# Kernel optimization log

Hardware: AMD Instinct MI355X
Metric: run time of the kernel (lower is better)

The kernel has to match this reference:

```python
import jax, jax.numpy as jnp
import numpy as np

DIM = 1024
SEQ_LEN = 4096
K_RANK = 256
HEADS = 16
HEAD_DIM = DIM // HEADS
BATCH = 4


def setup_inputs() -> dict:
    key = jax.random.key(0)
    k1, k2, k3, k4 = jax.random.split(key, 4)
    x = jax.random.normal(k1, (BATCH, SEQ_LEN, DIM), dtype=jnp.float32)
    W_qkv = jax.random.normal(k2, (DIM, 3 * DIM), dtype=jnp.float32) * (DIM ** -0.5)
    E = jax.random.normal(k3, (SEQ_LEN, K_RANK), dtype=jnp.float32)
    W_out = jax.random.normal(k4, (DIM, DIM), dtype=jnp.float32) * (DIM ** -0.5)
    b_out = jnp.zeros((DIM,), dtype=jnp.float32)
    return {"x": x, "W_qkv": W_qkv, "E": E, "W_out": W_out, "b_out": b_out}


def reference(x, W_qkv, E, W_out, b_out):
    B, N, D = x.shape
    scale = HEAD_DIM ** -0.5
    qkv = x @ W_qkv                                    # [B, N, 3D]
    q, k, v = jnp.split(qkv, 3, axis=-1)
    # [B, N, D] -> [B, H, N, hd]
    reshape_heads = lambda t: t.reshape(B, N, HEADS, HEAD_DIM).transpose(0, 2, 1, 3)
    q, k, v = map(reshape_heads, (q, k, v))
    # Linformer low-rank projection along sequence: [B, H, N, hd] -> [B, H, k, hd]
    k_proj = jnp.einsum('bhnd,nk->bhkd', k, E)
    v_proj = jnp.einsum('bhnd,nk->bhkd', v, E)
    scores = jnp.einsum('bhnd,bhkd->bhnk', q, k_proj) * scale  # [B, H, N, k]
    attn = jax.nn.softmax(scores, axis=-1)
    out = jnp.einsum('bhnk,bhkd->bhnd', attn, v_proj)  # [B, H, N, hd]
    out = out.transpose(0, 2, 1, 3).reshape(B, N, D)
    return out @ W_out + b_out
```

## Files before the change

### kernel.cpp

```cpp
#include <hip/hip_runtime.h>
#include <hip/hip_bf16.h>

typedef _Float16 f16;
typedef __attribute__((ext_vector_type(4))) _Float16 f16x4;
typedef __attribute__((ext_vector_type(8))) _Float16 f16x8;
typedef __attribute__((ext_vector_type(4))) float f32x4;

#define DIM 1024
#define SEQ 4096
#define KRNK 256
#define NH 16
#define HD 64
#define NB 4
#define ROWS (NB*SEQ)
#define NSPLIT 4

typedef const void __attribute__((address_space(1))) as1cv;
typedef void __attribute__((address_space(3))) as3v;

static __device__ __forceinline__ void glds16(const void* g, void* l) {
  __builtin_amdgcn_global_load_lds((as1cv*)g, (as3v*)l, 16, 0, 0);
}

template<int MODE>
__global__ __launch_bounds__(256) void k_prep_w(const float* __restrict__ in,
                                                f16* __restrict__ oh, f16* __restrict__ ol,
                                                int R, int C) {
  __shared__ float tile[64][65];
  int rtiles = R >> 6;
  int rt = blockIdx.x % rtiles, ct = blockIdx.x / rtiles;
  int r0 = rt << 6, c0 = ct << 6, t = threadIdx.x;
#pragma unroll
  for (int i = 0; i < 16; ++i) {
    int e = t + i * 256; int r = e >> 6, c = e & 63;
    tile[r][c] = in[(size_t)(r0 + r) * C + c0 + c];
  }
  __syncthreads();
#pragma unroll
  for (int i = 0; i < 16; ++i) {
    int e = t + i * 256; int c = e >> 6, r = e & 63;
    float v = tile[r][c];
    size_t idx = (size_t)(c0 + c) * R + r0 + r;
    if constexpr (MODE == 0) {
      v *= 256.0f;
      f16 h = (f16)v;
      oh[idx] = h;
      ol[idx] = (f16)(v - (float)h);
    } else {
      oh[idx] = (f16)v;
    }
  }
}

template<bool WH>
__global__ __launch_bounds__(256) void k_tsplit(const float* __restrict__ in,
                                                f16* __restrict__ oh,
                                                f16* __restrict__ oth,
                                                int R, int C) {
  __shared__ float tile[64][65];
  int rtiles = R >> 6;
  int rt = blockIdx.x % rtiles, ct = blockIdx.x / rtiles;
  int r0 = rt << 6, c0 = ct << 6, t = threadIdx.x;
  int cq = (t & 15) * 4, rr = t >> 4;
#pragma unroll
  for (int i = 0; i < 4; ++i) {
    int r = rr + i * 16;
    f32x4 v = *(const f32x4*)&in[(size_t)(r0 + r) * C + c0 + cq];
    tile[r][cq] = v[0]; tile[r][cq + 1] = v[1];
    tile[r][cq + 2] = v[2]; tile[r][cq + 3] = v[3];
    if constexpr (WH) {
      f16x4 h = {(f16)v[0], (f16)v[1], (f16)v[2], (f16)v[3]};
      *(f16x4*)&oh[(size_t)(r0 + r) * C + c0 + cq] = h;
    }
  }
  __syncthreads();
  int d4 = (t >> 4) * 4, sq = (t & 15) * 4;
#pragma unroll
  for (int j = 0; j < 4; ++j) {
    f16x4 h4;
#pragma unroll
    for (int k = 0; k < 4; ++k) h4[k] = (f16)tile[sq + k][d4 + j];
    *(f16x4*)&oth[(size_t)(c0 + d4 + j) * R + r0 + sq] = h4;
  }
}

template<bool ASPL, bool BSPL, int MT, int NT>
static __device__ __forceinline__ void mm_core(
    const f16* __restrict__ Ah, const f16* __restrict__ Al, int lda,
    const f16* __restrict__ Bh, const f16* __restrict__ Bl, int ldb,
    int bm, int bn, int K,
    f16* sAh, f16* sAl, f16* sBh, f16* sBl,
    f32x4 (&acc)[MT / 32][NT / 32]) {
  constexpr int MREP = MT / 32, NREP = NT / 32;
  constexpr int AI = MT / 32, BI = NT / 32;
  constexpr int ASZ = MT * 64, BSZ = NT * 64;
  const int t = threadIdx.x;
  const int lane = t & 63, w = t >> 6;
  const int wr = w >> 1, wc = w & 1;
  const int l15 = lane & 15, hi = lane >> 4;
  const f32x4 zero = {0.f, 0.f, 0.f, 0.f};
#pragma unroll
  for (int m = 0; m < MREP; ++m)
#pragma unroll
    for (int n = 0; n < NREP; ++n) acc[m][n] = zero;

  auto stage = [&](int kk, int bufi) {
#pragma unroll
    for (int i = 0; i < AI; ++i) {
      int c = t + i * 256;
      int row = c >> 3, cc = c & 7;
      size_t g = (size_t)(bm + row) * lda + kk + cc * 8;
      glds16(Ah + g, &sAh[bufi * ASZ + c * 8]);
      if constexpr (ASPL) glds16(Al + g, &sAl[bufi * ASZ + c * 8]);
    }
#pragma unroll
    for (int i = 0; i < BI; ++i) {
      int c = t + i * 256;
      int row = c >> 3, cc = c & 7;
      size_t g = (size_t)(bn + row) * ldb + kk + cc * 8;
      glds16(Bh + g, &sBh[bufi * BSZ + c * 8]);
      if constexpr (BSPL) glds16(Bl + g, &sBl[bufi * BSZ + c * 8]);
    }
  };

  stage(0, 0);
  int cur = 0;
  for (int kk = 0; kk < K; kk += 64) {
    __syncthreads();
    if (kk + 64 < K) stage(kk + 64, cur ^ 1);

    f16x8 avh[MREP][2], avl[MREP][2], bvh[NREP][2], bvl[NREP][2];
#pragma unroll
    for (int m = 0; m < MREP; ++m)
#pragma unroll
      for (int ks = 0; ks < 2; ++ks) {
        int off = cur * ASZ + (wr * (MT / 2) + m * 16 + l15) * 64 + ks * 32 + hi * 8;
        avh[m][ks] = *(const f16x8*)&sAh[off];
        if constexpr (ASPL) avl[m][ks] = *(const f16x8*)&sAl[off];
      }
#pragma unroll
    for (int n = 0; n < NREP; ++n)
#pragma unroll
      for (int ks = 0; ks < 2; ++ks) {
        int off = cur * BSZ + (wc * (NT / 2) + n * 16 + l15) * 64 + ks * 32 + hi * 8;
        bvh[n][ks] = *(const f16x8*)&sBh[off];
        if constexpr (BSPL) bvl[n][ks] = *(const f16x8*)&sBl[off];
      }
#pragma unroll
    for (int m = 0; m < MREP; ++m)
#pragma unroll
      for (int n = 0; n < NREP; ++n)
#pragma unroll
        for (int ks = 0; ks < 2; ++ks) {
          if constexpr (ASPL && BSPL) {
            acc[m][n] = __builtin_amdgcn_mfma_f32_16x16x32_f16(avl[m][ks], bvh[n][ks], acc[m][n], 0, 0, 0);
            acc[m][n] = __builtin_amdgcn_mfma_f32_16x16x32_f16(avh[m][ks], bvl[n][ks], acc[m][n], 0, 0, 0);
          } else if constexpr (BSPL) {
            acc[m][n] = __builtin_amdgcn_mfma_f32_16x16x32_f16(avh[m][ks], bvl[n][ks], acc[m][n], 0, 0, 0);
          }
          acc[m][n] = __builtin_amdgcn_mfma_f32_16x16x32_f16(avh[m][ks], bvh[n][ks], acc[m][n], 0, 0, 0);
        }
    cur ^= 1;
  }
}

__global__ __launch_bounds__(256) void k_xe2(const f16* __restrict__ Eth,
                                             const f16* __restrict__ xth,
                                             float* __restrict__ XEp) {
  __shared__ __align__(16) f16 sA[2 * 128 * 64];
  __shared__ __align__(16) f16 sB[2 * 64 * 64];
  int bx = blockIdx.x;
  int nt = bx & 15, mt = (bx >> 4) & 1, b = (bx >> 5) & 3, sp = bx >> 7;
  int bm = mt << 7, bn = nt << 6;
  int koff = sp * (SEQ / NSPLIT);
  f32x4 acc[4][2];
  mm_core<false, false, 128, 64>(Eth + koff, nullptr, SEQ,
                                 xth + (size_t)b * SEQ + koff, nullptr, ROWS,
                                 bm, bn, SEQ / NSPLIT, sA, nullptr, sB, nullptr, acc);
  const int t = threadIdx.x, lane = t & 63, w = t >> 6;
  const int wr = w >> 1, wc = w & 1, l15 = lane & 15, hi = lane >> 4;
#pragma unroll
  for (int m = 0; m < 4; ++m)
#pragma unroll
    for (int n = 0; n < 2; ++n)
#pragma unroll
      for (int r = 0; r < 4; ++r) {
        int kr = bm + wr * 64 + m * 16 + hi * 4 + r;
        int dd = bn + wc * 32 + n * 16 + l15;
        XEp[(((size_t)sp * NB + b) * KRNK + kr) * DIM + dd] = acc[m][n][r];
      }
}

__global__ __launch_bounds__(256) void k_xered(const float* __restrict__ XEp,
                                               f16* __restrict__ XEh,
                                               f16* __restrict__ XEl) {
  size_t i = (size_t)blockIdx.x * 256 + threadIdx.x;
  const size_t sstride = (size_t)NB * KRNK * DIM / 4;
  const f32x4* p = (const f32x4*)XEp;
  f32x4 s = p[i];
#pragma unroll
  for (int sp = 1; sp < NSPLIT; ++sp) s += p[i + sp * sstride];
  f16x4 h4, l4;
#pragma unroll
  for (int j = 0; j < 4; ++j) {
    f16 h = (f16)s[j];
    h4[j] = h;
    l4[j] = (f16)(s[j] - (float)h);
  }
  *(f16x4*)&XEh[i * 4] = h4;
  *(f16x4*)&XEl[i * 4] = l4;
}

static __device__ __forceinline__ void go_map(int bx, int& bm, int& bn) {
  int xcd = bx & 7, idx = bx >> 3;
  int nt = idx & 7, mt = xcd * 32 + (idx >> 3);
  bm = mt << 6;
  bn = nt << 7;
}

__global__ __launch_bounds__(256) void k_gq(const f16* __restrict__ xh,
                                            const f16* __restrict__ Wph,
                                            f16* __restrict__ q) {
  __shared__ __align__(16) f16 sA[2 * 64 * 64];
  __shared__ __align__(16) f16 sB[2 * 128 * 64];
  int bm, bn;
  go_map(blockIdx.x, bm, bn);
  f32x4 acc[2][4];
  mm_core<false, false, 64, 128>(xh, nullptr, DIM, Wph, nullptr, DIM, bm, bn, DIM,
                                 sA, nullptr, sB, nullptr, acc);
  const int t = threadIdx.x, lane = t & 63, w = t >> 6;
  const int wr = w >> 1, wc = w & 1, l15 = lane & 15, hi = lane >> 4;
#pragma unroll
  for (int m = 0; m < 2; ++m)
#pragma unroll
    for (int n = 0; n < 4; ++n)
#pragma unroll
      for (int r = 0; r < 4; ++r) {
        int row = bm + wr * 32 + m * 16 + hi * 4 + r;
        int col = bn + wc * 64 + n * 16 + l15;
        q[(size_t)row * DIM + col] = (f16)(acc[m][n][r] * (1.0f / 256.0f));
      }
}

__global__ __launch_bounds__(256) void k_t2(const f16* __restrict__ XEh,
                                            const f16* __restrict__ XEl,
                                            const f16* __restrict__ Wph,
                                            const f16* __restrict__ Wpl,
                                            f16* __restrict__ kph,
                                            f16* __restrict__ vpt) {
  __shared__ __align__(16) f16 sAh[2 * 128 * 64], sAl[2 * 128 * 64];
  __shared__ __align__(16) f16 sBh[2 * 64 * 64], sBl[2 * 64 * 64];
  int bx = blockIdx.x;
  int nt = bx & 15, mt = (bx >> 4) & 1, b = (bx >> 5) & 3, kv = bx >> 7;
  size_t abase = (size_t)b * KRNK * DIM;
  size_t wbase = (size_t)(DIM + kv * DIM) * DIM;
  f32x4 acc[4][2];
  mm_core<true, true, 128, 64>(XEh + abase, XEl + abase, DIM, Wph + wbase, Wpl + wbase, DIM,
                               mt << 7, nt << 6, DIM, sAh, sAl, sBh, sBl, acc);
  const int t = threadIdx.x, lane = t & 63, w = t >> 6;
  const int wr = w >> 1, wc = w & 1, l15 = lane & 15, hi = lane >> 4;
#pragma unroll
  for (int m = 0; m < 4; ++m)
#pragma unroll
    for (int n = 0; n < 2; ++n)
#pragma unroll
      for (int r = 0; r < 4; ++r) {
        int row = (mt << 7) + wr * 64 + m * 16 + hi * 4 + r;
        int col = (nt << 6) + wc * 32 + n * 16 + l15;
        float s = acc[m][n][r] * (1.0f / 256.0f);
        if (!kv) kph[((size_t)(b * KRNK + row)) * DIM + col] = (f16)s;
        else     vpt[((size_t)(b * DIM + col)) * KRNK + row] = (f16)s;
      }
}

__global__ __launch_bounds__(256) void k_attn(const f16* __restrict__ q,
                                              const f16* __restrict__ kph,
                                              const f16* __restrict__ vpt,
                                              f16* __restrict__ oattn) {
  __shared__ __align__(16) f16 sBuf[2][64 * 64];
  __shared__ __align__(16) f16 sP[64 * KRNK];
  int bx0 = blockIdx.x;
  int swz = (bx0 & 7) * 512 + (bx0 >> 3);
  int qb = swz & 63;
  int bh = swz >> 6;
  int b = bh >> 4, h = bh & 15;
  int t = threadIdx.x;
  int lane = t & 63, w = t >> 6;
  int l15 = lane & 15, hi = lane >> 4;

  const f16* kbase = kph + ((size_t)(b * KRNK)) * DIM + h * HD;
  const f16* vbase = vpt + ((size_t)(b * DIM + h * HD)) * KRNK;

  auto stageK = [&](int c, int bufi) {
#pragma unroll
    for (int i = 0; i < 2; ++i) {
      int sid = w * 128 + i * 64 + lane;
      int kr = sid >> 3, sl = sid & 7;
      glds16(kbase + (size_t)(c * 64 + kr) * DIM + ((sl ^ (kr & 7)) * 8),
             &sBuf[bufi][sid * 8]);
    }
  };
  auto stageV = [&](int c, int bufi) {
#pragma unroll
    for (int i = 0; i < 2; ++i) {
      int sid = w * 128 + i * 64 + lane;
      int hd = sid >> 3, sl = sid & 7;
      glds16(vbase + (size_t)hd * KRNK + c * 64 + ((sl ^ (hd & 7)) * 8),
             &sBuf[bufi][sid * 8]);
    }
  };

  int seqrow = qb * 64 + w * 16 + l15;
  const f16* qg = q + ((size_t)(b * SEQ + seqrow)) * DIM + h * HD;
  f16x8 aq[2];
  aq[0] = *(const f16x8*)(qg + hi * 8);
  aq[1] = *(const f16x8*)(qg + 32 + hi * 8);

  const f32x4 zero = {0.f, 0.f, 0.f, 0.f};
  f32x4 s[16];

  stageK(0, 0);
#pragma unroll
  for (int c = 0; c < 4; ++c) {
    __syncthreads();
    if (c < 3) stageK(c + 1, (c + 1) & 1);
    else       stageV(0, 0);
#pragma unroll
    for (int n = 0; n < 4; ++n) {
      int nn = c * 4 + n;
      s[nn] = zero;
      int krl = n * 16 + l15;
#pragma unroll
      for (int ks = 0; ks < 2; ++ks) {
        f16x8 bk = *(const f16x8*)&sBuf[c & 1][krl * 64 + (((ks * 4 + hi) ^ (krl & 7)) * 8)];
        s[nn] = __builtin_amdgcn_mfma_f32_16x16x32_f16(aq[ks], bk, s[nn], 0, 0, 0);
      }
    }
  }

  const float scale = 0.125f;
  float mx[4], sminv[4];
#pragma unroll
  for (int r = 0; r < 4; ++r) {
    float m0 = s[0][r];
#pragma unroll
    for (int n = 1; n < 16; ++n) m0 = fmaxf(m0, s[n][r]);
#pragma unroll
    for (int d = 1; d <= 8; d <<= 1) m0 = fmaxf(m0, __shfl_xor(m0, d));
    mx[r] = m0;
  }
  float sm[4] = {0.f, 0.f, 0.f, 0.f};
#pragma unroll
  for (int n = 0; n < 16; ++n)
#pragma unroll
    for (int r = 0; r < 4; ++r) {
      float p = __expf((s[n][r] - mx[r]) * scale);
      s[n][r] = p;
      sm[r] += p;
    }
#pragma unroll
  for (int r = 0; r < 4; ++r) {
    float t2 = sm[r];
#pragma unroll
    for (int d = 1; d <= 8; d <<= 1) t2 += __shfl_xor(t2, d);
    sminv[r] = 1.0f / t2;
  }

#pragma unroll
  for (int n = 0; n < 16; ++n)
#pragma unroll
    for (int r = 0; r < 4; ++r) {
      int qloc = w * 16 + hi * 4 + r;
      int kr = n * 16 + l15;
      int chunk = kr >> 3;
      sP[qloc * KRNK + ((chunk ^ (qloc & 7)) * 8) + (kr & 7)] = (f16)s[n][r];
    }

  f32x4 o[4];
#pragma unroll
  for (int n = 0; n < 4; ++n) o[n] = zero;
  int qloc = w * 16 + l15;
#pragma unroll
  for (int c = 0; c < 4; ++c) {
    __syncthreads();
    if (c < 3) stageV(c + 1, (c + 1) & 1);
#pragma unroll
    for (int sub = 0; sub < 2; ++sub) {
      int chunk = c * 8 + sub * 4 + hi;
      f16x8 pa = *(const f16x8*)&sP[qloc * KRNK + ((chunk ^ (qloc & 7)) * 8)];
#pragma unroll
      for (int n = 0; n < 4; ++n) {
        int hd = n * 16 + l15;
        f16x8 bv = *(const f16x8*)&sBuf[c & 1][hd * 64 + (((sub * 4 + hi) ^ (hd & 7)) * 8)];
        o[n] = __builtin_amdgcn_mfma_f32_16x16x32_f16(pa, bv, o[n], 0, 0, 0);
      }
    }
  }

  size_t obase = ((size_t)(b * SEQ + qb * 64)) * DIM + h * HD;
#pragma unroll
  for (int n = 0; n < 4; ++n)
#pragma unroll
    for (int r = 0; r < 4; ++r) {
      int qloc2 = w * 16 + hi * 4 + r;
      int hd = n * 16 + l15;
      oattn[obase + (size_t)qloc2 * DIM + hd] = (f16)(o[n][r] * sminv[r]);
    }
}

__global__ __launch_bounds__(256) void k_go(const f16* __restrict__ oattn,
                                            const f16* __restrict__ WoT,
                                            const float* __restrict__ bias,
                                            float* __restrict__ out) {
  __shared__ __align__(16) f16 sA[2 * 64 * 64];
  __shared__ __align__(16) f16 sB[2 * 128 * 64];
  int bm, bn;
  go_map(blockIdx.x, bm, bn);
  f32x4 acc[2][4];
  mm_core<false, false, 64, 128>(oattn, nullptr, DIM, WoT, nullptr, DIM, bm, bn, DIM,
                                 sA, nullptr, sB, nullptr, acc);
  const int t = threadIdx.x, lane = t & 63, w = t >> 6;
  const int wr = w >> 1, wc = w & 1, l15 = lane & 15, hi = lane >> 4;
#pragma unroll
  for (int m = 0; m < 2; ++m)
#pragma unroll
    for (int n = 0; n < 4; ++n)
#pragma unroll
      for (int r = 0; r < 4; ++r) {
        int row = bm + wr * 32 + m * 16 + hi * 4 + r;
        int col = bn + wc * 64 + n * 16 + l15;
        out[(size_t)row * DIM + col] = acc[m][n][r] + bias[col];
      }
}

extern "C" void kernel_launch(void* const* d_in, const int* in_sizes, int n_in,
                              void* d_out, int out_size, void* d_ws, size_t ws_size,
                              hipStream_t stream) {
  const float* x    = (const float*)d_in[0];
  const float* Wqkv = (const float*)d_in[1];
  const float* E    = (const float*)d_in[2];
  const float* Wout = (const float*)d_in[3];
  const float* bout = (const float*)d_in[4];
  float* out = (float*)d_out;

  char* p = (char*)d_ws;
  f16* Wph = (f16*)p;  p += (size_t)2 * 3 * DIM * DIM;
  f16* Wpl = (f16*)p;  p += (size_t)2 * 3 * DIM * DIM;
  f16* WoT = (f16*)p;  p += (size_t)2 * DIM * DIM;
  f16* xh  = (f16*)p;  p += (size_t)2 * ROWS * DIM;
  f16* xth = (f16*)p;  p += (size_t)2 * DIM * ROWS;
  f16* Eth = (f16*)p;  p += (size_t)2 * KRNK * SEQ;
  f16* XEh = (f16*)p;  p += (size_t)2 * NB * KRNK * DIM;
  f16* XEl = (f16*)p;  p += (size_t)2 * NB * KRNK * DIM;
  f16* kph = (f16*)p;  p += (size_t)2 * NB * KRNK * DIM;
  f16* vpt = (f16*)p;  p += (size_t)2 * NB * DIM * KRNK;
  f16* oattn = (f16*)p; p += (size_t)2 * ROWS * DIM;
  float* XEp = (float*)p;  p += (size_t)4 * NSPLIT * NB * KRNK * DIM;
  size_t need = (size_t)(p - (char*)d_ws);
  if (ws_size < need) return;

  f16* q = xth;

  k_prep_w<0><<<(DIM / 64) * (3 * DIM / 64), 256, 0, stream>>>(Wqkv, Wph, Wpl, DIM, 3 * DIM);
  k_prep_w<1><<<(DIM / 64) * (DIM / 64), 256, 0, stream>>>(Wout, WoT, nullptr, DIM, DIM);
  k_tsplit<true><<<(ROWS / 64) * (DIM / 64), 256, 0, stream>>>(x, xh, xth, ROWS, DIM);
  k_tsplit<false><<<(SEQ / 64) * (KRNK / 64), 256, 0, stream>>>(E, nullptr, Eth, SEQ, KRNK);
  k_xe2<<<512, 256, 0, stream>>>(Eth, xth, XEp);
  k_xered<<<(NB * KRNK * DIM / 4) / 256, 256, 0, stream>>>(XEp, XEh, XEl);
  k_gq<<<2048, 256, 0, stream>>>(xh, Wph, q);
  k_t2<<<256, 256, 0, stream>>>(XEh, XEl, Wph, Wpl, kph, vpt);
  k_attn<<<64 * 64, 256, 0, stream>>>(q, kph, vpt, oattn);
  k_go<<<2048, 256, 0, stream>>>(oattn, WoT, bout, out);
}
```

Baseline: 263.6 us.

## Fuse Q projection GEMM into attention kernel, dropping separate q kernel

```diff
diff --git a/kernel.cpp b/kernel.cpp
--- a/kernel.cpp
+++ b/kernel.cpp
@@ -209,37 +209,6 @@
   }
   *(f16x4*)&XEh[i * 4] = h4;
   *(f16x4*)&XEl[i * 4] = l4;
-}
-
-static __device__ __forceinline__ void go_map(int bx, int& bm, int& bn) {
-  int xcd = bx & 7, idx = bx >> 3;
-  int nt = idx & 7, mt = xcd * 32 + (idx >> 3);
-  bm = mt << 6;
-  bn = nt << 7;
-}
-
-__global__ __launch_bounds__(256) void k_gq(const f16* __restrict__ xh,
-                                            const f16* __restrict__ Wph,
-                                            f16* __restrict__ q) {
-  __shared__ __align__(16) f16 sA[2 * 64 * 64];
-  __shared__ __align__(16) f16 sB[2 * 128 * 64];
-  int bm, bn;
-  go_map(blockIdx.x, bm, bn);
-  f32x4 acc[2][4];
-  mm_core<false, false, 64, 128>(xh, nullptr, DIM, Wph, nullptr, DIM, bm, bn, DIM,
-                                 sA, nullptr, sB, nullptr, acc);
-  const int t = threadIdx.x, lane = t & 63, w = t >> 6;
-  const int wr = w >> 1, wc = w & 1, l15 = lane & 15, hi = lane >> 4;
-#pragma unroll
-  for (int m = 0; m < 2; ++m)
-#pragma unroll
-    for (int n = 0; n < 4; ++n)
-#pragma unroll
-      for (int r = 0; r < 4; ++r) {
-        int row = bm + wr * 32 + m * 16 + hi * 4 + r;
-        int col = bn + wc * 64 + n * 16 + l15;
-        q[(size_t)row * DIM + col] = (f16)(acc[m][n][r] * (1.0f / 256.0f));
-      }
 }
 
 __global__ __launch_bounds__(256) void k_t2(const f16* __restrict__ XEh,
@@ -273,28 +242,94 @@
       }
 }
 
-__global__ __launch_bounds__(256) void k_attn(const f16* __restrict__ q,
-                                              const f16* __restrict__ kph,
-                                              const f16* __restrict__ vpt,
-                                              f16* __restrict__ oattn) {
+__global__ __launch_bounds__(256) void k_fattn(const f16* __restrict__ xh,
+                                               const f16* __restrict__ Wph,
+                                               const f16* __restrict__ kph,
+                                               const f16* __restrict__ vpt,
+                                               f16* __restrict__ oattn) {
   __shared__ __align__(16) f16 sBuf[2][64 * 64];
   __shared__ __align__(16) f16 sP[64 * KRNK];
-  int bx0 = blockIdx.x;
-  int swz = (bx0 & 7) * 512 + (bx0 >> 3);
-  int qb = swz & 63;
-  int bh = swz >> 6;
+  int bx = blockIdx.x;
+  int xcd = bx & 7, i = bx >> 3;
+  int qb = xcd * 8 + (i >> 6);
+  int bh = i & 63;
   int b = bh >> 4, h = bh & 15;
   int t = threadIdx.x;
   int lane = t & 63, w = t >> 6;
   int l15 = lane & 15, hi = lane >> 4;
 
+  f16* sQA = sP;
+  f16* sQ  = sP + 8192;
+
+  const f16* Arow = xh + ((size_t)(b * SEQ + qb * 64)) * DIM;
+  const f16* Brow = Wph + ((size_t)(h * HD)) * DIM;
+
+  auto stageQ = [&](int kk, int bufi) {
+#pragma unroll
+    for (int i2 = 0; i2 < 2; ++i2) {
+      int sid = w * 128 + i2 * 64 + lane;
+      int row = sid >> 3, sl = sid & 7;
+      size_t g = (size_t)row * DIM + kk + ((sl ^ (row & 7)) * 8);
+      glds16(Arow + g, &sQA[bufi * 4096 + sid * 8]);
+      glds16(Brow + g, &sBuf[bufi][sid * 8]);
+    }
+  };
+
+  const f32x4 zero = {0.f, 0.f, 0.f, 0.f};
+  {
+    f32x4 qa[4];
+#pragma unroll
+    for (int n = 0; n < 4; ++n) qa[n] = zero;
+    stageQ(0, 0);
+    int cur = 0;
+    int arow = w * 16 + l15;
+    for (int kk = 0; kk < DIM; kk += 64) {
+      __syncthreads();
+      if (kk + 64 < DIM) stageQ(kk + 64, cur ^ 1);
+      f16x8 av[2], bv2[4][2];
+#pragma unroll
+      for (int ks = 0; ks < 2; ++ks)
+        av[ks] = *(const f16x8*)&sQA[cur * 4096 + arow * 64 + (((ks * 4 + hi) ^ (arow & 7)) * 8)];
+#pragma unroll
+      for (int n = 0; n < 4; ++n) {
+        int brow = n * 16 + l15;
+#pragma unroll
+        for (int ks = 0; ks < 2; ++ks)
+          bv2[n][ks] = *(const f16x8*)&sBuf[cur][brow * 64 + (((ks * 4 + hi) ^ (brow & 7)) * 8)];
+      }
+#pragma unroll
+      for (int n = 0; n < 4; ++n)
+#pragma unroll
+        for (int ks = 0; ks < 2; ++ks)
+          qa[n] = __builtin_amdgcn_mfma_f32_16x16x32_f16(av[ks], bv2[n][ks], qa[n], 0, 0, 0);
+      cur ^= 1;
+    }
+#pragma unroll
+    for (int n = 0; n < 4; ++n)
+#pragma unroll
+      for (int r = 0; r < 4; ++r) {
+        int qrow = w * 16 + hi * 4 + r;
+        int col = n * 16 + l15;
+        sQ[qrow * 64 + (((col >> 3) ^ (qrow & 7)) * 8) + (col & 7)] =
+            (f16)(qa[n][r] * (1.0f / 256.0f));
+      }
+  }
+  __syncthreads();
+
+  f16x8 aq[2];
+  {
+    int arow = w * 16 + l15;
+    aq[0] = *(const f16x8*)&sQ[arow * 64 + (((0 * 4 + hi) ^ (arow & 7)) * 8)];
+    aq[1] = *(const f16x8*)&sQ[arow * 64 + (((1 * 4 + hi) ^ (arow & 7)) * 8)];
+  }
+
   const f16* kbase = kph + ((size_t)(b * KRNK)) * DIM + h * HD;
   const f16* vbase = vpt + ((size_t)(b * DIM + h * HD)) * KRNK;
 
   auto stageK = [&](int c, int bufi) {
 #pragma unroll
-    for (int i = 0; i < 2; ++i) {
-      int sid = w * 128 + i * 64 + lane;
+    for (int i2 = 0; i2 < 2; ++i2) {
+      int sid = w * 128 + i2 * 64 + lane;
       int kr = sid >> 3, sl = sid & 7;
       glds16(kbase + (size_t)(c * 64 + kr) * DIM + ((sl ^ (kr & 7)) * 8),
              &sBuf[bufi][sid * 8]);
@@ -302,23 +337,15 @@
   };
   auto stageV = [&](int c, int bufi) {
 #pragma unroll
-    for (int i = 0; i < 2; ++i) {
-      int sid = w * 128 + i * 64 + lane;
+    for (int i2 = 0; i2 < 2; ++i2) {
+      int sid = w * 128 + i2 * 64 + lane;
       int hd = sid >> 3, sl = sid & 7;
       glds16(vbase + (size_t)hd * KRNK + c * 64 + ((sl ^ (hd & 7)) * 8),
              &sBuf[bufi][sid * 8]);
     }
   };
 
-  int seqrow = qb * 64 + w * 16 + l15;
-  const f16* qg = q + ((size_t)(b * SEQ + seqrow)) * DIM + h * HD;
-  f16x8 aq[2];
-  aq[0] = *(const f16x8*)(qg + hi * 8);
-  aq[1] = *(const f16x8*)(qg + 32 + hi * 8);
-
-  const f32x4 zero = {0.f, 0.f, 0.f, 0.f};
   f32x4 s[16];
-
   stageK(0, 0);
 #pragma unroll
   for (int c = 0; c < 4; ++c) {
@@ -406,6 +433,13 @@
       int hd = n * 16 + l15;
       oattn[obase + (size_t)qloc2 * DIM + hd] = (f16)(o[n][r] * sminv[r]);
     }
+}
+
+static __device__ __forceinline__ void go_map(int bx, int& bm, int& bn) {
+  int xcd = bx & 7, idx = bx >> 3;
+  int nt = idx & 7, mt = xcd * 32 + (idx >> 3);
+  bm = mt << 6;
+  bn = nt << 7;
 }
 
 __global__ __launch_bounds__(256) void k_go(const f16* __restrict__ oattn,
@@ -459,16 +493,13 @@
   size_t need = (size_t)(p - (char*)d_ws);
   if (ws_size < need) return;
 
-  f16* q = xth;
-
   k_prep_w<0><<<(DIM / 64) * (3 * DIM / 64), 256, 0, stream>>>(Wqkv, Wph, Wpl, DIM, 3 * DIM);
   k_prep_w<1><<<(DIM / 64) * (DIM / 64), 256, 0, stream>>>(Wout, WoT, nullptr, DIM, DIM);
   k_tsplit<true><<<(ROWS / 64) * (DIM / 64), 256, 0, stream>>>(x, xh, xth, ROWS, DIM);
   k_tsplit<false><<<(SEQ / 64) * (KRNK / 64), 256, 0, stream>>>(E, nullptr, Eth, SEQ, KRNK);
   k_xe2<<<512, 256, 0, stream>>>(Eth, xth, XEp);
   k_xered<<<(NB * KRNK * DIM / 4) / 256, 256, 0, stream>>>(XEp, XEh, XEl);
-  k_gq<<<2048, 256, 0, stream>>>(xh, Wph, q);
   k_t2<<<256, 256, 0, stream>>>(XEh, XEl, Wph, Wpl, kph, vpt);
-  k_attn<<<64 * 64, 256, 0, stream>>>(q, kph, vpt, oattn);
+  k_fattn<<<64 * 64, 256, 0, stream>>>(xh, Wph, kph, vpt, oattn);
   k_go<<<2048, 256, 0, stream>>>(oattn, WoT, bout, out);
 }
```

Result: slower. 327.1 us (+24.1%).
